# Kernel optimization log

Measured on AMD Instinct MI355X. Metric: run time of the kernel, lower is better.

Reference implementation:

```python
import jax, jax.numpy as jnp
import numpy as np

D_MODEL = 1024
D_STATE = 16
D_CONV = 4
EXPAND = 2
D_INNER = EXPAND * D_MODEL          # 2048
DT_RANK = D_MODEL // 16             # 64 (ceil(d_model/16))
B, L = 2, 2048


def setup_inputs() -> dict:
    key = jax.random.key(0)
    ks = jax.random.split(key, 8)
    s = 0.02
    return {
        "x": jax.random.normal(ks[0], (B, L, D_MODEL), jnp.float32),
        "ln_w": jnp.ones((D_MODEL,), jnp.float32),
        "ln_b": jnp.zeros((D_MODEL,), jnp.float32),
        "W_in": jax.random.normal(ks[1], (2 * D_INNER, D_MODEL), jnp.float32) * s,
        "conv_w": jax.random.normal(ks[2], (D_INNER, 1, D_CONV), jnp.float32) * s,
        "conv_b": jnp.zeros((D_INNER,), jnp.float32),
        "W_xproj": jax.random.normal(ks[3], (DT_RANK + 2 * D_STATE, D_INNER), jnp.float32) * s,
        "W_dt": jax.random.normal(ks[4], (D_INNER, DT_RANK), jnp.float32) * s,
        "b_dt": jax.random.normal(ks[5], (D_INNER,), jnp.float32) * 0.1,
        "A_log": jnp.log(jnp.broadcast_to(
            jnp.arange(1, D_STATE + 1, dtype=jnp.float32), (D_INNER, D_STATE))),
        "D_skip": jnp.ones((D_INNER,), jnp.float32),
        "W_out": jax.random.normal(ks[6], (D_MODEL, D_INNER), jnp.float32) * s,
    }


def reference(x, ln_w, ln_b, W_in, conv_w, conv_b, W_xproj, W_dt, b_dt,
              A_log, D_skip, W_out):
    # --- LayerNorm ---
    mu = jnp.mean(x, -1, keepdims=True)
    var = jnp.var(x, -1, keepdims=True)
    xn = (x - mu) * jax.lax.rsqrt(var + 1e-5) * ln_w + ln_b

    # --- in_proj -> (x_ssm, z gate) ---
    xz = jnp.einsum('bld,ed->ble', xn, W_in)          # [B,L,2*D_INNER]
    xs, z = jnp.split(xz, 2, axis=-1)                 # each [B,L,D_INNER]

    # --- depthwise causal conv1d + SiLU ---
    xc = jnp.transpose(xs, (0, 2, 1))                 # [B,D_INNER,L]
    xc = jax.lax.conv_general_dilated(
        xc, conv_w, window_strides=(1,), padding=[(D_CONV - 1, 0)],
        dimension_numbers=('NCH', 'OIH', 'NCH'),
        feature_group_count=D_INNER)
    xc = xc + conv_b[None, :, None]
    xs = jax.nn.silu(jnp.transpose(xc, (0, 2, 1)))    # [B,L,D_INNER]

    # --- input-dependent SSM params ---
    x_dbl = jnp.einsum('bld,ed->ble', xs, W_xproj)    # [B,L,DT_RANK+2*D_STATE]
    dt, Bm, Cm = jnp.split(x_dbl, [DT_RANK, DT_RANK + D_STATE], axis=-1)
    dt = jax.nn.softplus(jnp.einsum('blr,dr->bld', dt, W_dt) + b_dt)  # [B,L,D_INNER]

    A = -jnp.exp(A_log)                               # [D_INNER,D_STATE]
    deltaA = jnp.exp(dt[..., None] * A)               # [B,L,D_INNER,D_STATE]
    deltaBx = dt[..., None] * Bm[:, :, None, :] * xs[..., None]

    # --- selective scan over time ---
    def step(h, inp):
        dA, dBx, C = inp                              # [B,Din,S],[B,Din,S],[B,S]
        h = dA * h + dBx
        y = jnp.einsum('bds,bs->bd', h, C)
        return h, y

    h0 = jnp.zeros((x.shape[0], D_INNER, D_STATE), xs.dtype)
    _, ys = jax.lax.scan(step, h0, (jnp.moveaxis(deltaA, 1, 0),
                                    jnp.moveaxis(deltaBx, 1, 0),
                                    jnp.moveaxis(Cm, 1, 0)))
    y = jnp.moveaxis(ys, 0, 1) + xs * D_skip          # [B,L,D_INNER]

    # --- gate + out_proj + residual ---
    y = y * jax.nn.silu(z)
    out = jnp.einsum('bld,ed->ble', y, W_out)         # [B,L,D_MODEL]
    return x + out
```

## Files before the change

kernel.cpp:

```cpp
#include <hip/hip_runtime.h>
#include <hip/hip_bf16.h>


typedef __attribute__((ext_vector_type(4))) float f32x4;
typedef __attribute__((ext_vector_type(8))) short s16x8;

static __device__ __forceinline__ float b2f(ushort u) {
  union { float f; unsigned int i; } v; v.i = ((unsigned int)u) << 16; return v.f;
}
static __device__ __forceinline__ ushort f2b(float f) {
  union { __hip_bfloat16 h; ushort u; } v; v.h = __float2bfloat16(f); return v.u;
}

#define GLD16(gp, lp) __builtin_amdgcn_global_load_lds( \
    (const __attribute__((address_space(1))) void*)(gp), \
    (__attribute__((address_space(3))) void*)(lp), 16, 0, 0)

__global__ void prep_weights_kernel(const float* __restrict__ W_in,
    const float* __restrict__ W_out, const float* __restrict__ W_dt,
    const float* __restrict__ W_xproj, ushort* __restrict__ win,
    ushort* __restrict__ wout, ushort* __restrict__ wdt, ushort* __restrict__ wxp) {
  int i = blockIdx.x * 256 + threadIdx.x;
  if (i < 1048576) {
    float4 v = ((const float4*)W_in)[i];
    ((ushort4*)win)[i] = make_ushort4(f2b(v.x), f2b(v.y), f2b(v.z), f2b(v.w));
    return;
  }
  i -= 1048576;
  if (i < 524288) {
    float4 v = ((const float4*)W_out)[i];
    ((ushort4*)wout)[i] = make_ushort4(f2b(v.x), f2b(v.y), f2b(v.z), f2b(v.w));
    return;
  }
  i -= 524288;
  if (i < 32768) {
    float4 v = ((const float4*)W_dt)[i];
    ((ushort4*)wdt)[i] = make_ushort4(f2b(v.x), f2b(v.y), f2b(v.z), f2b(v.w));
    return;
  }
  i -= 32768;
  if (i < 65536) {
    int e  = i >> 9;
    int k4 = (i & 511) << 2;
    ushort4 o = make_ushort4(0, 0, 0, 0);
    if (e < 96) {
      float4 v = *(const float4*)(W_xproj + (size_t)e * 2048 + k4);
      o = make_ushort4(f2b(v.x), f2b(v.y), f2b(v.z), f2b(v.w));
    }
    ((ushort4*)wxp)[i] = o;
  }
}

__global__ __launch_bounds__(256) void ln_kernel(const float* __restrict__ x,
    const float* __restrict__ w, const float* __restrict__ b, ushort* __restrict__ xn) {
  const int row = blockIdx.x;
  const int tid = threadIdx.x;
  float4 v = ((const float4*)(x + (size_t)row * 1024))[tid];
  float s  = v.x + v.y + v.z + v.w;
  float s2 = v.x*v.x + v.y*v.y + v.z*v.z + v.w*v.w;
  #pragma unroll
  for (int off = 32; off; off >>= 1) { s += __shfl_xor(s, off); s2 += __shfl_xor(s2, off); }
  __shared__ float red[8];
  if ((tid & 63) == 0) { red[tid >> 6] = s; red[(tid >> 6) + 4] = s2; }
  __syncthreads();
  float S  = red[0] + red[1] + red[2] + red[3];
  float S2 = red[4] + red[5] + red[6] + red[7];
  float mu   = S * (1.0f / 1024.0f);
  float var  = S2 * (1.0f / 1024.0f) - mu * mu;
  float rstd = rsqrtf(var + 1e-5f);
  float4 wv = ((const float4*)w)[tid];
  float4 bv = ((const float4*)b)[tid];
  ushort4 o = make_ushort4(
      f2b((v.x - mu) * rstd * wv.x + bv.x),
      f2b((v.y - mu) * rstd * wv.y + bv.y),
      f2b((v.z - mu) * rstd * wv.z + bv.z),
      f2b((v.w - mu) * rstd * wv.w + bv.w));
  ((ushort4*)(xn + (size_t)row * 1024))[tid] = o;
}

template<int EPI, int BM>
__global__ __launch_bounds__(256, 2) void gemm_lds(
    const ushort* __restrict__ A, const ushort* __restrict__ B,
    float* __restrict__ Cf, ushort* __restrict__ Cb,
    const float* __restrict__ aux,
    int M, int N, int K, int kt_per)
{
  constexpr int MF  = BM / 32;
  constexpr int RSH = (BM == 128) ? 6 : 5;
  __shared__ __align__(16) char SM[16896];
  ushort* As = (ushort*)SM;
  ushort* Bs = (ushort*)(SM + BM * 64);
  float*  epi = (float*)SM;
  const int tid  = threadIdx.x;
  const int lane = tid & 63;
  const int wid  = tid >> 6;
  const int wr = wid >> 1, wc = wid & 1;
  const int m0 = blockIdx.x * BM, n0 = blockIdx.y * 128;
  const int kt0 = blockIdx.z * kt_per;

  const int srow = tid >> 2;
  const int scol = (tid & 3) << 3;
  const ushort* Ag0 = A + (size_t)(m0 + srow) * K + scol + (size_t)kt0 * 32;
  const ushort* Ag1 = Ag0 + (size_t)64 * K;
  const ushort* Bg0 = B + (size_t)(n0 + srow) * K + scol + (size_t)kt0 * 32;
  const ushort* Bg1 = Bg0 + (size_t)64 * K;
  char* ldsA0 = (char*)As + wid * 1024;
  char* ldsA1 = (char*)As + 4096 + wid * 1024;
  char* ldsB0 = (char*)Bs + wid * 1024;
  char* ldsB1 = (char*)Bs + 4096 + wid * 1024;

  f32x4 acc[MF][4];
  #pragma unroll
  for (int m = 0; m < MF; ++m)
    #pragma unroll
    for (int n = 0; n < 4; ++n)
      acc[m][n] = (f32x4){0.f, 0.f, 0.f, 0.f};

  const int frow = lane & 15;
  const int fk   = (lane >> 4) << 3;
  const ushort* AsR = As + (wr * (BM / 2) + frow) * 32 + fk;
  const ushort* BsR = Bs + (wc * 64 + frow) * 32 + fk;

  for (int kt = 0; kt < kt_per; ++kt) {
    const size_t ko = (size_t)kt * 32;
    GLD16(Ag0 + ko, ldsA0);
    if constexpr (BM == 128) GLD16(Ag1 + ko, ldsA1);
    GLD16(Bg0 + ko, ldsB0);
    GLD16(Bg1 + ko, ldsB1);
    __syncthreads();
    s16x8 af[MF], bfr[4];
    #pragma unroll
    for (int m = 0; m < MF; ++m) af[m] = *(const s16x8*)(AsR + m * 512);
    #pragma unroll
    for (int n = 0; n < 4; ++n) bfr[n] = *(const s16x8*)(BsR + n * 512);
    #pragma unroll
    for (int m = 0; m < MF; ++m)
      #pragma unroll
      for (int n = 0; n < 4; ++n)
        acc[m][n] = __builtin_amdgcn_mfma_f32_16x16x32_bf16(af[m], bfr[n], acc[m][n], 0, 0, 0);
    __syncthreads();
  }

  const int rl = tid >> 3;
  const int c0 = (tid & 7) << 4;
  const size_t zoff = (EPI == 2) ? (size_t)blockIdx.z * M * N : 0;
  #pragma unroll
  for (int m = 0; m < MF; ++m) {
    #pragma unroll
    for (int n = 0; n < 4; ++n) {
      const int cl = wc * 64 + n * 16 + (lane & 15);
      #pragma unroll
      for (int j = 0; j < 4; ++j) {
        const int rr = wr * 16 + ((lane >> 4) << 2) + j;
        epi[rr * 132 + cl] = acc[m][n][j];
      }
    }
    __syncthreads();
    const int grow = m0 + ((rl >> 4) << RSH) + m * 16 + (rl & 15);
    const int gcol = n0 + c0;
    float v[16];
    #pragma unroll
    for (int q = 0; q < 16; ++q) v[q] = epi[rl * 132 + c0 + q];
    if (EPI == 1) {
      ushort u[16];
      #pragma unroll
      for (int q = 0; q < 16; ++q) u[q] = f2b(v[q]);
      *(int4*)(Cb + (size_t)grow * N + gcol)     = *(int4*)&u[0];
      *(int4*)(Cb + (size_t)grow * N + gcol + 8) = *(int4*)&u[8];
    } else if (EPI == 2) {
      #pragma unroll
      for (int q = 0; q < 4; ++q)
        *(float4*)(Cf + zoff + (size_t)grow * N + gcol + q * 4) = *(float4*)&v[q * 4];
    } else if (EPI == 3) {
      ushort u[16];
      #pragma unroll
      for (int q = 0; q < 4; ++q) {
        float4 bb = *(const float4*)(aux + gcol + q * 4);
        float t0 = v[q*4+0] + bb.x, t1 = v[q*4+1] + bb.y;
        float t2 = v[q*4+2] + bb.z, t3 = v[q*4+3] + bb.w;
        u[q*4+0] = f2b(fmaxf(t0, 0.f) + __logf(1.f + __expf(-fabsf(t0))));
        u[q*4+1] = f2b(fmaxf(t1, 0.f) + __logf(1.f + __expf(-fabsf(t1))));
        u[q*4+2] = f2b(fmaxf(t2, 0.f) + __logf(1.f + __expf(-fabsf(t2))));
        u[q*4+3] = f2b(fmaxf(t3, 0.f) + __logf(1.f + __expf(-fabsf(t3))));
      }
      *(int4*)(Cb + (size_t)grow * N + gcol)     = *(int4*)&u[0];
      *(int4*)(Cb + (size_t)grow * N + gcol + 8) = *(int4*)&u[8];
    } else {
      #pragma unroll
      for (int q = 0; q < 4; ++q) {
        float4 rr2 = *(const float4*)(aux + (size_t)grow * N + gcol + q * 4);
        float4 ov = make_float4(rr2.x + v[q*4+0], rr2.y + v[q*4+1],
                                rr2.z + v[q*4+2], rr2.w + v[q*4+3]);
        *(float4*)(Cf + (size_t)grow * N + gcol + q * 4) = ov;
      }
    }
    __syncthreads();
  }
}

__global__ __launch_bounds__(256) void conv_silu_kernel(const ushort* __restrict__ xz,
    const float* __restrict__ cw, const float* __restrict__ cb, ushort* __restrict__ xs) {
  const int idx = blockIdx.x * 256 + threadIdx.x;
  const int d4 = idx & 511;
  const int lg = (idx >> 9) & 511;
  const int b  = idx >> 18;
  const int d  = d4 << 2;
  const int l0 = lg << 2;
  float w[4][4];
  const float* cwd = cw + d * 4;
  #pragma unroll
  for (int j = 0; j < 4; ++j)
    #pragma unroll
    for (int t = 0; t < 4; ++t) w[j][t] = cwd[j * 4 + t];
  const float4 bias = *(const float4*)(cb + d);
  float vin[7][4];
  const size_t base = (size_t)(b * 2048) * 4096 + d;
  #pragma unroll
  for (int j = 0; j < 7; ++j) {
    const int ls = l0 - 3 + j;
    if (ls >= 0) {
      ushort4 xv = *(const ushort4*)(xz + base + (size_t)ls * 4096);
      vin[j][0] = b2f(xv.x); vin[j][1] = b2f(xv.y);
      vin[j][2] = b2f(xv.z); vin[j][3] = b2f(xv.w);
    } else {
      vin[j][0] = vin[j][1] = vin[j][2] = vin[j][3] = 0.f;
    }
  }
  #pragma unroll
  for (int i = 0; i < 4; ++i) {
    float a0 = bias.x, a1 = bias.y, a2 = bias.z, a3 = bias.w;
    #pragma unroll
    for (int t = 0; t < 4; ++t) {
      a0 += vin[i + t][0] * w[0][t];
      a1 += vin[i + t][1] * w[1][t];
      a2 += vin[i + t][2] * w[2][t];
      a3 += vin[i + t][3] * w[3][t];
    }
    ushort4 o;
    o.x = f2b(a0 / (1.f + __expf(-a0)));
    o.y = f2b(a1 / (1.f + __expf(-a1)));
    o.z = f2b(a2 / (1.f + __expf(-a2)));
    o.w = f2b(a3 / (1.f + __expf(-a3)));
    *(ushort4*)(xs + (size_t)(b * 2048 + l0 + i) * 2048 + d) = o;
  }
}

__global__ __launch_bounds__(256) void xdbl_reduce_kernel(const float* __restrict__ x8,
    float* __restrict__ xdbl, ushort* __restrict__ dtlow) {
  const int i = blockIdx.x * 256 + threadIdx.x;
  const int r = i >> 5, c4 = (i & 31) << 2;
  float4 s = make_float4(0.f, 0.f, 0.f, 0.f);
  #pragma unroll
  for (int z = 0; z < 8; ++z) {
    float4 v = *(const float4*)(x8 + (size_t)z * 524288 + (size_t)r * 128 + c4);
    s.x += v.x; s.y += v.y; s.z += v.z; s.w += v.w;
  }
  *(float4*)(xdbl + (size_t)r * 128 + c4) = s;
  if (c4 < 64) {
    ((ushort4*)(dtlow + (size_t)r * 64))[c4 >> 2] =
        make_ushort4(f2b(s.x), f2b(s.y), f2b(s.z), f2b(s.w));
  }
}

__global__ __launch_bounds__(256, 4) void scanA_kernel(const ushort* __restrict__ dt,
    const ushort* __restrict__ xs, const float* __restrict__ xdbl,
    const float* __restrict__ A_log, float* __restrict__ FH, float* __restrict__ Sdt) {
  __shared__ float Bsh[32 * 16];
  const int tid = threadIdx.x;
  const int d = blockIdx.x * 256 + tid;
  const int c = blockIdx.y, b = blockIdx.z;
  const int t0 = b * 2048 + c * 32;
  if (tid < 128) {
    const int il = tid >> 2, q = (tid & 3) << 2;
    *(float4*)&Bsh[il * 16 + q] = *(const float4*)(xdbl + (size_t)(t0 + il) * 128 + 64 + q);
  }
  float Ad[16];
  #pragma unroll
  for (int s = 0; s < 16; ++s) Ad[s] = -__expf(A_log[(size_t)d * 16 + s]);
  __syncthreads();
  float h[16];
  #pragma unroll
  for (int s = 0; s < 16; ++s) h[s] = 0.f;
  float sdt = 0.f;
  const ushort* dtp = dt + (size_t)t0 * 2048 + d;
  const ushort* xsp = xs + (size_t)t0 * 2048 + d;
  float dtv = b2f(dtp[0]);
  float xv  = b2f(xsp[0]);
  for (int il = 0; il < 32; ++il) {
    float dtn = 0.f, xn = 0.f;
    if (il < 31) { dtn = b2f(dtp[(il + 1) * 2048]); xn = b2f(xsp[(il + 1) * 2048]); }
    const float dx = dtv * xv;
    sdt += dtv;
    const float* Bv = &Bsh[il * 16];
    #pragma unroll
    for (int s = 0; s < 16; ++s) h[s] = __expf(dtv * Ad[s]) * h[s] + dx * Bv[s];
    dtv = dtn; xv = xn;
  }
  const size_t fo = (((size_t)b * 64 + c) * 2048 + d) * 16;
  #pragma unroll
  for (int q = 0; q < 4; ++q)
    *(float4*)(FH + fo + q * 4) = make_float4(h[q*4], h[q*4+1], h[q*4+2], h[q*4+3]);
  Sdt[((size_t)b * 64 + c) * 2048 + d] = sdt;
}

__global__ __launch_bounds__(256) void scanB_kernel(float* __restrict__ FH,
    const float* __restrict__ Sdt, const float* __restrict__ A_log) {
  const int idx = blockIdx.x * 256 + threadIdx.x;
  const int s = idx & 15;
  const int d = (idx >> 4) & 2047;
  const int b = idx >> 15;
  const float Ad = -__expf(A_log[(size_t)d * 16 + s]);
  float H = 0.f;
  #pragma unroll 8
  for (int c = 0; c < 64; ++c) {
    const size_t o = (((size_t)b * 64 + c) * 2048 + d) * 16 + s;
    const float F   = FH[o];
    const float sdt = Sdt[((size_t)b * 64 + c) * 2048 + d];
    FH[o] = H;
    H = __expf(sdt * Ad) * H + F;
  }
}

__global__ __launch_bounds__(256, 4) void scanC_kernel(const ushort* __restrict__ dt,
    const ushort* __restrict__ xs, const float* __restrict__ xdbl,
    const ushort* __restrict__ xz, const float* __restrict__ A_log,
    const float* __restrict__ Dskip, const float* __restrict__ FH,
    ushort* __restrict__ yg) {
  __shared__ float BCsh[32 * 32];
  const int tid = threadIdx.x;
  const int d = blockIdx.x * 256 + tid;
  const int c = blockIdx.y, b = blockIdx.z;
  const int t0 = b * 2048 + c * 32;
  {
    const int il = tid >> 3, q = (tid & 7) << 2;
    *(float4*)&BCsh[il * 32 + q] = *(const float4*)(xdbl + (size_t)(t0 + il) * 128 + 64 + q);
  }
  float Ad[16];
  #pragma unroll
  for (int s = 0; s < 16; ++s) Ad[s] = -__expf(A_log[(size_t)d * 16 + s]);
  float h[16];
  const size_t ho = (((size_t)b * 64 + c) * 2048 + d) * 16;
  {
    const float4* Hp = (const float4*)(FH + ho);
    float4 H0 = Hp[0], H1 = Hp[1], H2 = Hp[2], H3 = Hp[3];
    h[0]=H0.x; h[1]=H0.y; h[2]=H0.z; h[3]=H0.w;
    h[4]=H1.x; h[5]=H1.y; h[6]=H1.z; h[7]=H1.w;
    h[8]=H2.x; h[9]=H2.y; h[10]=H2.z; h[11]=H2.w;
    h[12]=H3.x; h[13]=H3.y; h[14]=H3.z; h[15]=H3.w;
  }
  __syncthreads();
  const float Dk = Dskip[d];
  const ushort* dtp = dt + (size_t)t0 * 2048 + d;
  const ushort* xsp = xs + (size_t)t0 * 2048 + d;
  const ushort* zp  = xz + (size_t)t0 * 4096 + 2048 + d;
  ushort* ygp = yg + (size_t)t0 * 2048 + d;
  float dtv = b2f(dtp[0]);
  float xv  = b2f(xsp[0]);
  float zv  = b2f(zp[0]);
  for (int il = 0; il < 32; ++il) {
    float dtn = 0.f, xn = 0.f, zn = 0.f;
    if (il < 31) {
      dtn = b2f(dtp[(il + 1) * 2048]);
      xn  = b2f(xsp[(il + 1) * 2048]);
      zn  = b2f(zp[(size_t)(il + 1) * 4096]);
    }
    const float dx = dtv * xv;
    const float* Bv = &BCsh[il * 32];
    const float* Cv = &BCsh[il * 32 + 16];
    float y = 0.f;
    #pragma unroll
    for (int s = 0; s < 16; ++s) {
      h[s] = __expf(dtv * Ad[s]) * h[s] + dx * Bv[s];
      y += h[s] * Cv[s];
    }
    const float g = zv / (1.f + __expf(-zv));
    ygp[il * 2048] = f2b((y + xv * Dk) * g);
    dtv = dtn; xv = xn; zv = zn;
  }
}

extern "C" void kernel_launch(void* const* d_in, const int* in_sizes, int n_in,
                              void* d_out, int out_size, void* d_ws, size_t ws_size,
                              hipStream_t stream) {
  (void)in_sizes; (void)n_in; (void)out_size; (void)ws_size;
  const float* x       = (const float*)d_in[0];
  const float* ln_w    = (const float*)d_in[1];
  const float* ln_b    = (const float*)d_in[2];
  const float* W_in    = (const float*)d_in[3];
  const float* conv_w  = (const float*)d_in[4];
  const float* conv_b  = (const float*)d_in[5];
  const float* W_xproj = (const float*)d_in[6];
  const float* W_dt    = (const float*)d_in[7];
  const float* b_dt    = (const float*)d_in[8];
  const float* A_log   = (const float*)d_in[9];
  const float* D_skip  = (const float*)d_in[10];
  const float* W_out   = (const float*)d_in[11];
  float* out = (float*)d_out;

  char* ws = (char*)d_ws;
  size_t off = 0;
  auto alloc = [&](size_t bytes) -> void* {
    void* p = ws + off;
    off += (bytes + 255) & ~(size_t)255;
    return p;
  };
  ushort* win_bf   = (ushort*)alloc((size_t)4096 * 1024 * 2);
  ushort* wout_bf  = (ushort*)alloc((size_t)1024 * 2048 * 2);
  ushort* wxp_bf   = (ushort*)alloc((size_t)128 * 2048 * 2);
  ushort* wdt_bf   = (ushort*)alloc((size_t)2048 * 64 * 2);
  ushort* xn_bf    = (ushort*)alloc((size_t)4096 * 1024 * 2);
  ushort* xz_bf    = (ushort*)alloc((size_t)4096 * 4096 * 2);
  ushort* xs_bf    = (ushort*)alloc((size_t)4096 * 2048 * 2);
  float*  xdbl     = (float*)alloc((size_t)4096 * 128 * 4);
  float*  xdbl8    = (float*)alloc((size_t)8 * 4096 * 128 * 4);
  ushort* dtlow_bf = (ushort*)alloc((size_t)4096 * 64 * 2);
  ushort* dtf_bf   = (ushort*)alloc((size_t)4096 * 2048 * 2);
  float*  SdtBuf   = (float*)alloc((size_t)2 * 64 * 2048 * 4);
  ushort* yg_bf    = (ushort*)alloc((size_t)4096 * 2048 * 2);
  float*  FH       = xdbl8;

  prep_weights_kernel<<<6528, 256, 0, stream>>>(W_in, W_out, W_dt, W_xproj,
                                                win_bf, wout_bf, wdt_bf, wxp_bf);
  ln_kernel<<<4096, 256, 0, stream>>>(x, ln_w, ln_b, xn_bf);

  gemm_lds<1, 128><<<dim3(32, 32, 1), 256, 0, stream>>>(xn_bf, win_bf, nullptr, xz_bf,
                                                        nullptr, 4096, 4096, 1024, 32);
  conv_silu_kernel<<<2048, 256, 0, stream>>>(xz_bf, conv_w, conv_b, xs_bf);

  gemm_lds<2, 64><<<dim3(64, 1, 8), 256, 0, stream>>>(xs_bf, wxp_bf, xdbl8, nullptr,
                                                      nullptr, 4096, 128, 2048, 8);
  xdbl_reduce_kernel<<<512, 256, 0, stream>>>(xdbl8, xdbl, dtlow_bf);

  gemm_lds<3, 64><<<dim3(64, 16, 1), 256, 0, stream>>>(dtlow_bf, wdt_bf, nullptr, dtf_bf,
                                                       b_dt, 4096, 2048, 64, 2);

  scanA_kernel<<<dim3(8, 64, 2), 256, 0, stream>>>(dtf_bf, xs_bf, xdbl, A_log, FH, SdtBuf);
  scanB_kernel<<<256, 256, 0, stream>>>(FH, SdtBuf, A_log);
  scanC_kernel<<<dim3(8, 64, 2), 256, 0, stream>>>(dtf_bf, xs_bf, xdbl, xz_bf, A_log, D_skip,
                                                   FH, yg_bf);

  gemm_lds<4, 64><<<dim3(64, 8, 1), 256, 0, stream>>>(yg_bf, wout_bf, out, nullptr, x,
                                                      4096, 1024, 2048, 64);
}
```

Before: 302.6 us.

## Double-buffer GEMM LDS tiles with BK=64 and XOR-swizzled layout

```diff
diff --git a/kernel.cpp b/kernel.cpp
--- a/kernel.cpp
+++ b/kernel.cpp
@@ -78,74 +78,90 @@
   ((ushort4*)(xn + (size_t)row * 1024))[tid] = o;
 }
 
-template<int EPI, int BM>
-__global__ __launch_bounds__(256, 2) void gemm_lds(
+template<int EPI>
+__global__ __launch_bounds__(256, 2) void gemm_db(
     const ushort* __restrict__ A, const ushort* __restrict__ B,
     float* __restrict__ Cf, ushort* __restrict__ Cb,
     const float* __restrict__ aux,
     int M, int N, int K, int kt_per)
 {
-  constexpr int MF  = BM / 32;
-  constexpr int RSH = (BM == 128) ? 6 : 5;
-  __shared__ __align__(16) char SM[16896];
-  ushort* As = (ushort*)SM;
-  ushort* Bs = (ushort*)(SM + BM * 64);
-  float*  epi = (float*)SM;
+  __shared__ __align__(16) char SM[49152];
   const int tid  = threadIdx.x;
   const int lane = tid & 63;
   const int wid  = tid >> 6;
   const int wr = wid >> 1, wc = wid & 1;
-  const int m0 = blockIdx.x * BM, n0 = blockIdx.y * 128;
+  const int m0 = blockIdx.x * 64, n0 = blockIdx.y * 128;
   const int kt0 = blockIdx.z * kt_per;
 
-  const int srow = tid >> 2;
-  const int scol = (tid & 3) << 3;
-  const ushort* Ag0 = A + (size_t)(m0 + srow) * K + scol + (size_t)kt0 * 32;
-  const ushort* Ag1 = Ag0 + (size_t)64 * K;
-  const ushort* Bg0 = B + (size_t)(n0 + srow) * K + scol + (size_t)kt0 * 32;
-  const ushort* Bg1 = Bg0 + (size_t)64 * K;
-  char* ldsA0 = (char*)As + wid * 1024;
-  char* ldsA1 = (char*)As + 4096 + wid * 1024;
-  char* ldsB0 = (char*)Bs + wid * 1024;
-  char* ldsB1 = (char*)Bs + 4096 + wid * 1024;
-
-  f32x4 acc[MF][4];
-  #pragma unroll
-  for (int m = 0; m < MF; ++m)
+  const int srow = tid >> 3;
+  const int sxor = ((tid & 7) ^ (srow & 7)) << 3;
+  const ushort* Ag = A + (size_t)(m0 + srow) * K + sxor + (size_t)kt0 * 64;
+  const ushort* Bg = B + (size_t)(n0 + srow) * K + sxor + (size_t)kt0 * 64;
+  const size_t rstep = (size_t)32 * K;
+  char* lds0 = (char*)SM + wid * 1024;
+
+  f32x4 acc[2][4];
+  #pragma unroll
+  for (int m = 0; m < 2; ++m)
     #pragma unroll
     for (int n = 0; n < 4; ++n)
       acc[m][n] = (f32x4){0.f, 0.f, 0.f, 0.f};
 
   const int frow = lane & 15;
   const int fk   = (lane >> 4) << 3;
-  const ushort* AsR = As + (wr * (BM / 2) + frow) * 32 + fk;
-  const ushort* BsR = Bs + (wc * 64 + frow) * 32 + fk;
-
-  for (int kt = 0; kt < kt_per; ++kt) {
-    const size_t ko = (size_t)kt * 32;
-    GLD16(Ag0 + ko, ldsA0);
-    if constexpr (BM == 128) GLD16(Ag1 + ko, ldsA1);
-    GLD16(Bg0 + ko, ldsB0);
-    GLD16(Bg1 + ko, ldsB1);
+  const int sw   = (lane & 7) << 3;
+
+#define STAGE(sel, ktv) { \
+    const ushort* ag = Ag + (size_t)(ktv) * 64; \
+    const ushort* bg = Bg + (size_t)(ktv) * 64; \
+    char* ba = lds0 + (sel) * 24576; \
+    GLD16(ag,             ba); \
+    GLD16(ag + rstep,     ba + 4096); \
+    GLD16(bg,             ba + 8192); \
+    GLD16(bg + rstep,     ba + 12288); \
+    GLD16(bg + 2 * rstep, ba + 16384); \
+    GLD16(bg + 3 * rstep, ba + 20480); \
+  }
+
+#define COMPUTE(sel) { \
+    const ushort* Asb = (const ushort*)((const char*)SM + (sel) * 24576); \
+    const ushort* Bsb = Asb + 4096;  \
+    _Pragma("unroll") \
+    for (int kk = 0; kk < 2; ++kk) { \
+      const int col = (kk * 32 + fk) ^ sw; \
+      s16x8 af[2], bf[4]; \
+      _Pragma("unroll") \
+      for (int m = 0; m < 2; ++m) \
+        af[m] = *(const s16x8*)(Asb + (wr * 32 + m * 16 + frow) * 64 + col); \
+      _Pragma("unroll") \
+      for (int n = 0; n < 4; ++n) \
+        bf[n] = *(const s16x8*)(Bsb + (wc * 64 + n * 16 + frow) * 64 + col); \
+      _Pragma("unroll") \
+      for (int m = 0; m < 2; ++m) \
+        _Pragma("unroll") \
+        for (int n = 0; n < 4; ++n) \
+          acc[m][n] = __builtin_amdgcn_mfma_f32_16x16x32_bf16(af[m], bf[n], acc[m][n], 0, 0, 0); \
+    } \
+  }
+
+  STAGE(0, 0);
+  __syncthreads();
+  int c = 0;
+  for (int kt = 0; kt < kt_per - 1; ++kt) {
+    STAGE(c ^ 1, kt + 1);
+    COMPUTE(c);
     __syncthreads();
-    s16x8 af[MF], bfr[4];
-    #pragma unroll
-    for (int m = 0; m < MF; ++m) af[m] = *(const s16x8*)(AsR + m * 512);
-    #pragma unroll
-    for (int n = 0; n < 4; ++n) bfr[n] = *(const s16x8*)(BsR + n * 512);
-    #pragma unroll
-    for (int m = 0; m < MF; ++m)
-      #pragma unroll
-      for (int n = 0; n < 4; ++n)
-        acc[m][n] = __builtin_amdgcn_mfma_f32_16x16x32_bf16(af[m], bfr[n], acc[m][n], 0, 0, 0);
-    __syncthreads();
-  }
-
+    c ^= 1;
+  }
+  COMPUTE(c);
+  __syncthreads();
+
+  float* epi = (float*)SM;
   const int rl = tid >> 3;
   const int c0 = (tid & 7) << 4;
   const size_t zoff = (EPI == 2) ? (size_t)blockIdx.z * M * N : 0;
   #pragma unroll
-  for (int m = 0; m < MF; ++m) {
+  for (int m = 0; m < 2; ++m) {
     #pragma unroll
     for (int n = 0; n < 4; ++n) {
       const int cl = wc * 64 + n * 16 + (lane & 15);
@@ -156,7 +172,7 @@
       }
     }
     __syncthreads();
-    const int grow = m0 + ((rl >> 4) << RSH) + m * 16 + (rl & 15);
+    const int grow = m0 + ((rl >> 4) << 5) + m * 16 + (rl & 15);
     const int gcol = n0 + c0;
     float v[16];
     #pragma unroll
@@ -196,6 +212,8 @@
     }
     __syncthreads();
   }
+#undef STAGE
+#undef COMPUTE
 }
 
 __global__ __launch_bounds__(256) void conv_silu_kernel(const ushort* __restrict__ xz,
@@ -423,22 +441,22 @@
                                                 win_bf, wout_bf, wdt_bf, wxp_bf);
   ln_kernel<<<4096, 256, 0, stream>>>(x, ln_w, ln_b, xn_bf);
 
-  gemm_lds<1, 128><<<dim3(32, 32, 1), 256, 0, stream>>>(xn_bf, win_bf, nullptr, xz_bf,
-                                                        nullptr, 4096, 4096, 1024, 32);
+  gemm_db<1><<<dim3(64, 32, 1), 256, 0, stream>>>(xn_bf, win_bf, nullptr, xz_bf,
+                                                  nullptr, 4096, 4096, 1024, 16);
   conv_silu_kernel<<<2048, 256, 0, stream>>>(xz_bf, conv_w, conv_b, xs_bf);
 
-  gemm_lds<2, 64><<<dim3(64, 1, 8), 256, 0, stream>>>(xs_bf, wxp_bf, xdbl8, nullptr,
-                                                      nullptr, 4096, 128, 2048, 8);
+  gemm_db<2><<<dim3(64, 1, 8), 256, 0, stream>>>(xs_bf, wxp_bf, xdbl8, nullptr,
+                                                 nullptr, 4096, 128, 2048, 4);
   xdbl_reduce_kernel<<<512, 256, 0, stream>>>(xdbl8, xdbl, dtlow_bf);
 
-  gemm_lds<3, 64><<<dim3(64, 16, 1), 256, 0, stream>>>(dtlow_bf, wdt_bf, nullptr, dtf_bf,
-                                                       b_dt, 4096, 2048, 64, 2);
+  gemm_db<3><<<dim3(64, 16, 1), 256, 0, stream>>>(dtlow_bf, wdt_bf, nullptr, dtf_bf,
+                                                  b_dt, 4096, 2048, 64, 1);
 
   scanA_kernel<<<dim3(8, 64, 2), 256, 0, stream>>>(dtf_bf, xs_bf, xdbl, A_log, FH, SdtBuf);
   scanB_kernel<<<256, 256, 0, stream>>>(FH, SdtBuf, A_log);
   scanC_kernel<<<dim3(8, 64, 2), 256, 0, stream>>>(dtf_bf, xs_bf, xdbl, xz_bf, A_log, D_skip,
                                                    FH, yg_bf);
 
-  gemm_lds<4, 64><<<dim3(64, 8, 1), 256, 0, stream>>>(yg_bf, wout_bf, out, nullptr, x,
-                                                      4096, 1024, 2048, 64);
-}
+  gemm_db<4><<<dim3(64, 8, 1), 256, 0, stream>>>(yg_bf, wout_bf, out, nullptr, x,
+                                                 4096, 1024, 2048, 32);
+}
```

After: 290.7 us. -3.9%, faster.
